# Kernel optimization log

Measured on AMD Instinct MI355X. Metric: run time of the kernel, lower is better.

Reference implementation:

```python
import jax, jax.numpy as jnp
import numpy as np

ALPHA = 1.0

def setup_inputs() -> dict:
    key = jax.random.key(0)
    kz, kc = jax.random.split(key)
    N, K, D = 65536, 256, 256
    z = jax.random.normal(kz, (N, D), dtype=jnp.float32)
    centroids = jax.random.normal(kc, (K, D), dtype=jnp.float32)
    return {"z": z, "centroids": centroids}

def reference(z, centroids):
    # squared euclidean distances (N, K) via expansion; same math as
    # sum((z[:,None,:]-c)**2, -1) without the (N,K,D) intermediate
    z2 = jnp.sum(z * z, axis=1, keepdims=True)            # (N, 1)
    c2 = jnp.sum(centroids * centroids, axis=1)           # (K,)
    sse = jnp.maximum(z2 + c2[None, :] - 2.0 * (z @ centroids.T), 0.0)
    # Student-t kernel
    q = (1.0 + sse / ALPHA) ** (-(ALPHA + 1.0) / 2.0)
    q = q / jnp.sum(q, axis=1, keepdims=True)             # row normalize
    # target distribution p
    sf = q * q / jnp.sum(q, axis=0, keepdims=True)        # col normalize of q^2
    p = sf / jnp.sum(sf, axis=1, keepdims=True)           # row normalize
    return (p, q)
```

## Files before the change

### kernel.cpp

```cpp
#include <hip/hip_runtime.h>
#include <stdint.h>

#define N_ROWS 65536
#define K_CENT 256
#define D_DIM  256

typedef __attribute__((ext_vector_type(8))) short bf16x8;
typedef __attribute__((ext_vector_type(4))) float f32x4;

__device__ __forceinline__ float bf2f(unsigned short u) {
    union { unsigned int i; float f; } v;
    v.i = ((unsigned int)u) << 16;
    return v.f;
}

__device__ __forceinline__ unsigned short f2bf(float f) {
    union { float f; unsigned int i; } v;
    v.f = f;
    unsigned int r = (v.i + 0x7FFFu + ((v.i >> 16) & 1u)) >> 16;
    return (unsigned short)r;
}

__global__ void c2_kernel(const float* __restrict__ cent,
                          float* __restrict__ c2,
                          unsigned short* __restrict__ cent_bf) {
    int row  = blockIdx.x;
    int lane = threadIdx.x;
    const float4 v = *(const float4*)(cent + (size_t)row * D_DIM + lane * 4);
    unsigned short b0 = f2bf(v.x), b1 = f2bf(v.y), b2 = f2bf(v.z), b3 = f2bf(v.w);
    ushort4 bv; bv.x = b0; bv.y = b1; bv.z = b2; bv.w = b3;
    *(ushort4*)(cent_bf + (size_t)row * D_DIM + lane * 4) = bv;
    float f0 = bf2f(b0), f1 = bf2f(b1), f2 = bf2f(b2), f3 = bf2f(b3);
    float s = f0 * f0 + f1 * f1 + f2 * f2 + f3 * f3;
    #pragma unroll
    for (int off = 32; off >= 1; off >>= 1) s += __shfl_xor(s, off, 64);
    if (lane == 0) c2[row] = s;
}

__global__ __launch_bounds__(256, 4) void pass1_kernel(
        const float* __restrict__ z,
        const unsigned short* __restrict__ cent_bf,
        const float* __restrict__ c2,
        float* __restrict__ partials,
        float* __restrict__ q_out) {
    __shared__ __align__(16) unsigned short bstage[64 * D_DIM];
    __shared__ float col_lds[4][K_CENT];

    const int tid  = threadIdx.x;
    const int wave = tid >> 6;
    const int lane = tid & 63;
    const int m15  = lane & 15;
    const int quad = lane >> 4;
    const int row0 = blockIdx.x * 64 + wave * 16;

    const float* za = z + (size_t)(row0 + m15) * D_DIM + quad * 8;
    float4 a[16];
    #pragma unroll
    for (int i = 0; i < 8; ++i) {
        a[2 * i]     = *(const float4*)(za + i * 32);
        a[2 * i + 1] = *(const float4*)(za + i * 32 + 4);
    }
    bf16x8 afrag[8];
    float z2p = 0.0f;
    #pragma unroll
    for (int ks = 0; ks < 8; ++ks) {
        const float av[8] = {a[2*ks].x, a[2*ks].y, a[2*ks].z, a[2*ks].w,
                             a[2*ks+1].x, a[2*ks+1].y, a[2*ks+1].z, a[2*ks+1].w};
        #pragma unroll
        for (int j = 0; j < 8; ++j) {
            unsigned short ub = f2bf(av[j]);
            afrag[ks][j] = (short)ub;
            float f = bf2f(ub);
            z2p += f * f;
        }
    }
    z2p += __shfl_xor(z2p, 16, 64);
    z2p += __shfl_xor(z2p, 32, 64);
    float z2r[4];
    #pragma unroll
    for (int r = 0; r < 4; ++r) z2r[r] = __shfl(z2p, quad * 4 + r, 64);

    f32x4 acc[16];
    #pragma unroll
    for (int t = 0; t < 16; ++t) acc[t] = (f32x4){0.f, 0.f, 0.f, 0.f};

    #pragma unroll
    for (int c = 0; c < 4; ++c) {
        const unsigned short* src = cent_bf + (size_t)c * 64 * D_DIM;
        #pragma unroll
        for (int h = 0; h < 2; ++h) {
            bf16x8 st[4];
            #pragma unroll
            for (int i = 0; i < 4; ++i) {
                int F  = (h * 4 + i) * 256 + tid;
                int qd = F & 3, mm = (F >> 2) & 15, tt = (F >> 6) & 3, kk = F >> 8;
                int s16 = tt * 512 + mm * 32 + kk * 4 + qd;
                st[i] = *(const bf16x8*)&src[s16 * 8];
            }
            #pragma unroll
            for (int i = 0; i < 4; ++i) {
                int F = (h * 4 + i) * 256 + tid;
                *(bf16x8*)&bstage[F * 8] = st[i];
            }
        }
        __syncthreads();
        #pragma unroll
        for (int ks = 0; ks < 8; ++ks) {
            #pragma unroll
            for (int t = 0; t < 4; ++t) {
                bf16x8 bfrag = *(const bf16x8*)&bstage[(ks * 256 + t * 64 + m15 * 4 + quad) * 8];
                acc[c * 4 + t] = __builtin_amdgcn_mfma_f32_16x16x32_bf16(
                    afrag[ks], bfrag, acc[c * 4 + t], 0, 0, 0);
            }
        }
        __syncthreads();
    }

    float rowsum[4] = {0.f, 0.f, 0.f, 0.f};
    #pragma unroll
    for (int t = 0; t < 16; ++t) {
        float c2v = c2[t * 16 + m15];
        #pragma unroll
        for (int r = 0; r < 4; ++r) {
            float sse = z2r[r] + c2v - 2.0f * acc[t][r];
            sse = fmaxf(sse, 0.0f);
            float u = 1.0f / (1.0f + sse);
            acc[t][r] = u;
            rowsum[r] += u;
        }
    }
    #pragma unroll
    for (int r = 0; r < 4; ++r) {
        float v = rowsum[r];
        v += __shfl_xor(v, 1, 64);
        v += __shfl_xor(v, 2, 64);
        v += __shfl_xor(v, 4, 64);
        v += __shfl_xor(v, 8, 64);
        rowsum[r] = 1.0f / v;
    }

    float colp[16];
    #pragma unroll
    for (int t = 0; t < 16; ++t) {
        float cp = 0.0f;
        #pragma unroll
        for (int r = 0; r < 4; ++r) {
            float qv = acc[t][r] * rowsum[r];
            cp += qv;
            q_out[(size_t)(row0 + quad * 4 + r) * K_CENT + t * 16 + m15] = qv;
        }
        cp += __shfl_xor(cp, 16, 64);
        cp += __shfl_xor(cp, 32, 64);
        colp[t] = cp;
    }
    if (quad == 0) {
        #pragma unroll
        for (int t = 0; t < 16; ++t) col_lds[wave][t * 16 + lane] = colp[t];
    }
    __syncthreads();
    float sp = col_lds[0][tid] + col_lds[1][tid] + col_lds[2][tid] + col_lds[3][tid];
    partials[(size_t)blockIdx.x * K_CENT + tid] = sp;
}

__global__ __launch_bounds__(256) void colsum_kernel(
        const float* __restrict__ partials,
        float* __restrict__ s_col) {
    const int tid = threadIdx.x;
    const float* base = partials + (size_t)blockIdx.x * 64 * K_CENT + tid;
    float s = 0.0f;
    #pragma unroll
    for (int h = 0; h < 8; ++h) {
        float v[8];
        #pragma unroll
        for (int i = 0; i < 8; ++i)
            v[i] = base[(h * 8 + i) * K_CENT];
        #pragma unroll
        for (int i = 0; i < 8; ++i) s += v[i];
    }
    atomicAdd(&s_col[tid], s);
}

__global__ __launch_bounds__(256) void pass2_kernel(
        const float* __restrict__ q,
        const float* __restrict__ s_col,
        float* __restrict__ p) {
    const int tid  = threadIdx.x;
    const int lane = tid & 63;
    const int wave = tid >> 6;
    const int wid  = blockIdx.x * 4 + wave;

    const float4 sv = *(const float4*)(s_col + lane * 4);
    const float is0 = 1.0f / sv.x, is1 = 1.0f / sv.y,
                is2 = 1.0f / sv.z, is3 = 1.0f / sv.w;

    const float* qb = q + (size_t)wid * 8 * K_CENT + lane * 4;
    float*       pb = p + (size_t)wid * 8 * K_CENT + lane * 4;

    float4 qv[8];
    #pragma unroll
    for (int r = 0; r < 8; ++r) qv[r] = *(const float4*)(qb + r * K_CENT);

    #pragma unroll
    for (int r = 0; r < 8; ++r) {
        float sf0 = qv[r].x * qv[r].x * is0;
        float sf1 = qv[r].y * qv[r].y * is1;
        float sf2 = qv[r].z * qv[r].z * is2;
        float sf3 = qv[r].w * qv[r].w * is3;
        float part = sf0 + sf1 + sf2 + sf3;
        #pragma unroll
        for (int off = 32; off >= 1; off >>= 1) part += __shfl_xor(part, off, 64);
        const float rinv = 1.0f / part;
        float4 ov;
        ov.x = sf0 * rinv; ov.y = sf1 * rinv;
        ov.z = sf2 * rinv; ov.w = sf3 * rinv;
        *(float4*)(pb + r * K_CENT) = ov;
    }
}

extern "C" void kernel_launch(void* const* d_in, const int* in_sizes, int n_in,
                              void* d_out, int out_size, void* d_ws, size_t ws_size,
                              hipStream_t stream) {
    const float* z    = (const float*)d_in[0];
    const float* cent = (const float*)d_in[1];
    float* p_out = (float*)d_out;
    float* q_out = p_out + (size_t)N_ROWS * K_CENT;

    float* c2       = (float*)d_ws;
    float* s_col    = c2 + K_CENT;
    unsigned short* cent_bf = (unsigned short*)(s_col + K_CENT);
    float* partials = (float*)(cent_bf + K_CENT * D_DIM);

    hipMemsetAsync(s_col, 0, K_CENT * sizeof(float), stream);
    c2_kernel<<<K_CENT, 64, 0, stream>>>(cent, c2, cent_bf);
    pass1_kernel<<<N_ROWS / 64, 256, 0, stream>>>(z, cent_bf, c2, partials, q_out);
    colsum_kernel<<<16, 256, 0, stream>>>(partials, s_col);
    pass2_kernel<<<N_ROWS / (4 * 8), 256, 0, stream>>>(q_out, s_col, p_out);
}
```

Baseline: 212.5 us.

## Fuse column reduction and p computation into pass1 via grid-wide barrier

Merges pass1, colsum and pass2 into one kernel. Blocks publish column partials and signal an atomic counter; the first 64 blocks reduce the partials into s_col once every block has arrived, and then all blocks spin until that reduction finishes. Each block then computes p from the q values still held in registers, so q is no longer read back from memory and two launches disappear. Centroid staging in LDS is halved to 32-row chunks so the block's LDS footprint shrinks, and the column scratch reuses that buffer. The spin barrier needs all 1024 blocks to be resident on the device at once, otherwise the kernel deadlocks.

```diff
diff --git a/kernel.cpp b/kernel.cpp
--- a/kernel.cpp
+++ b/kernel.cpp
@@ -4,6 +4,8 @@
 #define N_ROWS 65536
 #define K_CENT 256
 #define D_DIM  256
+#define GRID_BLOCKS (N_ROWS / 64)
+#define RED_BLOCKS  64
 
 typedef __attribute__((ext_vector_type(8))) short bf16x8;
 typedef __attribute__((ext_vector_type(4))) float f32x4;
@@ -19,6 +21,10 @@
     v.f = f;
     unsigned int r = (v.i + 0x7FFFu + ((v.i >> 16) & 1u)) >> 16;
     return (unsigned short)r;
+}
+
+__device__ __forceinline__ unsigned int agent_load(const unsigned int* p) {
+    return __hip_atomic_load(p, __ATOMIC_ACQUIRE, __HIP_MEMORY_SCOPE_AGENT);
 }
 
 __global__ void c2_kernel(const float* __restrict__ cent,
@@ -37,14 +43,16 @@
     if (lane == 0) c2[row] = s;
 }
 
-__global__ __launch_bounds__(256, 4) void pass1_kernel(
+__global__ __launch_bounds__(256, 4) void fused_kernel(
         const float* __restrict__ z,
         const unsigned short* __restrict__ cent_bf,
         const float* __restrict__ c2,
         float* __restrict__ partials,
-        float* __restrict__ q_out) {
-    __shared__ __align__(16) unsigned short bstage[64 * D_DIM];
-    __shared__ float col_lds[4][K_CENT];
+        float* __restrict__ s_col,
+        unsigned int* __restrict__ counters,
+        float* __restrict__ q_out,
+        float* __restrict__ p_out) {
+    __shared__ __align__(16) unsigned short bstage[32 * D_DIM];
 
     const int tid  = threadIdx.x;
     const int wave = tid >> 6;
@@ -85,32 +93,29 @@
     for (int t = 0; t < 16; ++t) acc[t] = (f32x4){0.f, 0.f, 0.f, 0.f};
 
     #pragma unroll
-    for (int c = 0; c < 4; ++c) {
-        const unsigned short* src = cent_bf + (size_t)c * 64 * D_DIM;
-        #pragma unroll
-        for (int h = 0; h < 2; ++h) {
-            bf16x8 st[4];
-            #pragma unroll
-            for (int i = 0; i < 4; ++i) {
-                int F  = (h * 4 + i) * 256 + tid;
-                int qd = F & 3, mm = (F >> 2) & 15, tt = (F >> 6) & 3, kk = F >> 8;
-                int s16 = tt * 512 + mm * 32 + kk * 4 + qd;
-                st[i] = *(const bf16x8*)&src[s16 * 8];
-            }
-            #pragma unroll
-            for (int i = 0; i < 4; ++i) {
-                int F = (h * 4 + i) * 256 + tid;
-                *(bf16x8*)&bstage[F * 8] = st[i];
-            }
+    for (int c = 0; c < 8; ++c) {
+        const unsigned short* src = cent_bf + (size_t)c * 32 * D_DIM;
+        bf16x8 st[4];
+        #pragma unroll
+        for (int i = 0; i < 4; ++i) {
+            int F  = i * 256 + tid;
+            int qd = F & 3, mm = (F >> 2) & 15, tt = (F >> 6) & 1, kk = F >> 7;
+            int s16 = tt * 512 + mm * 32 + kk * 4 + qd;
+            st[i] = *(const bf16x8*)&src[s16 * 8];
+        }
+        #pragma unroll
+        for (int i = 0; i < 4; ++i) {
+            int F = i * 256 + tid;
+            *(bf16x8*)&bstage[F * 8] = st[i];
         }
         __syncthreads();
         #pragma unroll
         for (int ks = 0; ks < 8; ++ks) {
             #pragma unroll
-            for (int t = 0; t < 4; ++t) {
-                bf16x8 bfrag = *(const bf16x8*)&bstage[(ks * 256 + t * 64 + m15 * 4 + quad) * 8];
-                acc[c * 4 + t] = __builtin_amdgcn_mfma_f32_16x16x32_bf16(
-                    afrag[ks], bfrag, acc[c * 4 + t], 0, 0, 0);
+            for (int t = 0; t < 2; ++t) {
+                bf16x8 bfrag = *(const bf16x8*)&bstage[(ks * 128 + t * 64 + m15 * 4 + quad) * 8];
+                acc[c * 2 + t] = __builtin_amdgcn_mfma_f32_16x16x32_bf16(
+                    afrag[ks], bfrag, acc[c * 2 + t], 0, 0, 0);
             }
         }
         __syncthreads();
@@ -146,6 +151,7 @@
         #pragma unroll
         for (int r = 0; r < 4; ++r) {
             float qv = acc[t][r] * rowsum[r];
+            acc[t][r] = qv;
             cp += qv;
             q_out[(size_t)(row0 + quad * 4 + r) * K_CENT + t * 16 + m15] = qv;
         }
@@ -153,67 +159,71 @@
         cp += __shfl_xor(cp, 32, 64);
         colp[t] = cp;
     }
+    float* col_lds = (float*)bstage;
     if (quad == 0) {
         #pragma unroll
-        for (int t = 0; t < 16; ++t) col_lds[wave][t * 16 + lane] = colp[t];
+        for (int t = 0; t < 16; ++t) col_lds[wave * K_CENT + t * 16 + lane] = colp[t];
     }
     __syncthreads();
-    float sp = col_lds[0][tid] + col_lds[1][tid] + col_lds[2][tid] + col_lds[3][tid];
+    float sp = col_lds[tid] + col_lds[K_CENT + tid] +
+               col_lds[2 * K_CENT + tid] + col_lds[3 * K_CENT + tid];
     partials[(size_t)blockIdx.x * K_CENT + tid] = sp;
-}
-
-__global__ __launch_bounds__(256) void colsum_kernel(
-        const float* __restrict__ partials,
-        float* __restrict__ s_col) {
-    const int tid = threadIdx.x;
-    const float* base = partials + (size_t)blockIdx.x * 64 * K_CENT + tid;
-    float s = 0.0f;
-    #pragma unroll
-    for (int h = 0; h < 8; ++h) {
-        float v[8];
-        #pragma unroll
-        for (int i = 0; i < 8; ++i)
-            v[i] = base[(h * 8 + i) * K_CENT];
-        #pragma unroll
-        for (int i = 0; i < 8; ++i) s += v[i];
-    }
-    atomicAdd(&s_col[tid], s);
-}
-
-__global__ __launch_bounds__(256) void pass2_kernel(
-        const float* __restrict__ q,
-        const float* __restrict__ s_col,
-        float* __restrict__ p) {
-    const int tid  = threadIdx.x;
-    const int lane = tid & 63;
-    const int wave = tid >> 6;
-    const int wid  = blockIdx.x * 4 + wave;
-
-    const float4 sv = *(const float4*)(s_col + lane * 4);
-    const float is0 = 1.0f / sv.x, is1 = 1.0f / sv.y,
-                is2 = 1.0f / sv.z, is3 = 1.0f / sv.w;
-
-    const float* qb = q + (size_t)wid * 8 * K_CENT + lane * 4;
-    float*       pb = p + (size_t)wid * 8 * K_CENT + lane * 4;
-
-    float4 qv[8];
-    #pragma unroll
-    for (int r = 0; r < 8; ++r) qv[r] = *(const float4*)(qb + r * K_CENT);
-
-    #pragma unroll
-    for (int r = 0; r < 8; ++r) {
-        float sf0 = qv[r].x * qv[r].x * is0;
-        float sf1 = qv[r].y * qv[r].y * is1;
-        float sf2 = qv[r].z * qv[r].z * is2;
-        float sf3 = qv[r].w * qv[r].w * is3;
-        float part = sf0 + sf1 + sf2 + sf3;
-        #pragma unroll
-        for (int off = 32; off >= 1; off >>= 1) part += __shfl_xor(part, off, 64);
-        const float rinv = 1.0f / part;
-        float4 ov;
-        ov.x = sf0 * rinv; ov.y = sf1 * rinv;
-        ov.z = sf2 * rinv; ov.w = sf3 * rinv;
-        *(float4*)(pb + r * K_CENT) = ov;
+
+    __threadfence();
+    __syncthreads();
+    if (tid == 0) atomicAdd(&counters[0], 1u);
+
+    if (blockIdx.x < RED_BLOCKS) {
+        if (tid == 0) {
+            while (agent_load(&counters[0]) < GRID_BLOCKS)
+                __builtin_amdgcn_s_sleep(2);
+        }
+        __syncthreads();
+        __threadfence();
+        const float* base = partials + (size_t)blockIdx.x * 16 * K_CENT + tid;
+        float s = 0.0f;
+        #pragma unroll
+        for (int h = 0; h < 16; ++h) s += base[h * K_CENT];
+        atomicAdd(&s_col[tid], s);
+        __threadfence();
+        __syncthreads();
+        if (tid == 0) atomicAdd(&counters[1], 1u);
+    }
+
+    if (tid == 0) {
+        while (agent_load(&counters[1]) < RED_BLOCKS)
+            __builtin_amdgcn_s_sleep(2);
+    }
+    __syncthreads();
+    __threadfence();
+
+    float rs2[4] = {0.f, 0.f, 0.f, 0.f};
+    #pragma unroll
+    for (int t = 0; t < 16; ++t) {
+        float inv_s = 1.0f / s_col[t * 16 + m15];
+        #pragma unroll
+        for (int r = 0; r < 4; ++r) {
+            float sf = acc[t][r] * acc[t][r] * inv_s;
+            acc[t][r] = sf;
+            rs2[r] += sf;
+        }
+    }
+    #pragma unroll
+    for (int r = 0; r < 4; ++r) {
+        float v = rs2[r];
+        v += __shfl_xor(v, 1, 64);
+        v += __shfl_xor(v, 2, 64);
+        v += __shfl_xor(v, 4, 64);
+        v += __shfl_xor(v, 8, 64);
+        rs2[r] = 1.0f / v;
+    }
+    #pragma unroll
+    for (int t = 0; t < 16; ++t) {
+        #pragma unroll
+        for (int r = 0; r < 4; ++r) {
+            p_out[(size_t)(row0 + quad * 4 + r) * K_CENT + t * 16 + m15] =
+                acc[t][r] * rs2[r];
+        }
     }
 }
 
@@ -225,14 +235,15 @@
     float* p_out = (float*)d_out;
     float* q_out = p_out + (size_t)N_ROWS * K_CENT;
 
-    float* c2       = (float*)d_ws;
-    float* s_col    = c2 + K_CENT;
-    unsigned short* cent_bf = (unsigned short*)(s_col + K_CENT);
-    float* partials = (float*)(cent_bf + K_CENT * D_DIM);
-
-    hipMemsetAsync(s_col, 0, K_CENT * sizeof(float), stream);
+    float* c2             = (float*)d_ws;
+    float* s_col          = c2 + K_CENT;
+    unsigned int* counters = (unsigned int*)(s_col + K_CENT);
+    unsigned short* cent_bf = (unsigned short*)(counters + 4);
+    float* partials       = (float*)(cent_bf + K_CENT * D_DIM);
+
+    hipMemsetAsync(s_col, 0, K_CENT * sizeof(float) + 4 * sizeof(unsigned int),
+                   stream);
     c2_kernel<<<K_CENT, 64, 0, stream>>>(cent, c2, cent_bf);
-    pass1_kernel<<<N_ROWS / 64, 256, 0, stream>>>(z, cent_bf, c2, partials, q_out);
-    colsum_kernel<<<16, 256, 0, stream>>>(partials, s_col);
-    pass2_kernel<<<N_ROWS / (4 * 8), 256, 0, stream>>>(q_out, s_col, p_out);
-}
+    fused_kernel<<<GRID_BLOCKS, 256, 0, stream>>>(
+        z, cent_bf, c2, partials, s_col, counters, q_out, p_out);
+}
```

After: 601.6 us. 2.83x slower.
